# Kernel optimization log

Measured on AMD Instinct MI355X. Metric: run time of the kernel, lower is better.

## Reference

```python
import jax, jax.numpy as jnp
import numpy as np

N_ENT = 4096
N_REL = 4
F = 128
BATCH = 8192
ADJ_DENSITY = 0.01


def setup_inputs() -> dict:
    key = jax.random.key(0)
    ks = jax.random.split(key, 8)
    features = jax.random.normal(ks[0], (N_ENT, F), dtype=jnp.float32)
    # sparse binary adjacency per relation (matches count_nonzero degree normalization)
    adj = (jax.random.uniform(ks[1], (N_REL, N_ENT, N_ENT)) < ADJ_DENSITY).astype(jnp.float32)
    W1 = jax.random.normal(ks[2], (N_REL, F, F), dtype=jnp.float32)  # [R, out, in]
    W2 = jax.random.normal(ks[3], (N_REL, F, F), dtype=jnp.float32)
    # DistMult init: diagonal relation matrices (full params, as in the torch code)
    diag_vals = jax.random.normal(ks[4], (N_REL, F), dtype=jnp.float32)
    relmats = jax.vmap(jnp.diag)(diag_vals)  # [R, F, F]
    e1_idx = jax.random.randint(ks[5], (BATCH,), 0, N_ENT)
    rel_idx = jax.random.randint(ks[6], (BATCH,), 0, N_REL)
    e2_idx = jax.random.randint(ks[7], (BATCH,), 0, N_ENT)
    return {"features": features, "adj": adj, "W1": W1, "W2": W2,
            "relmats": relmats, "e1_idx": e1_idx, "rel_idx": rel_idx, "e2_idx": e2_idx}


def _conv_layer(adj, feat, W):
    # degree normalization: 1 / count_nonzero(A_r, dim=1), zeros -> 1
    deg = jnp.sum(adj != 0, axis=2).astype(feat.dtype)            # [R, N]
    inv_deg = 1.0 / jnp.where(deg == 0, 1.0, deg)                 # [R, N]
    agg = jnp.einsum('rnm,mf->rnf', adj, feat)                    # [R, N, F_in]
    y = jnp.einsum('rnf,rof->rno', agg, W)                        # [R, N, F_out] (x @ W_r.T)
    y = jnp.sum(inv_deg[:, :, None] * y, axis=0)                  # [N, F_out]
    return jax.nn.sigmoid(y)


def reference(features, adj, W1, W2, relmats, e1_idx, rel_idx, e2_idx):
    h = _conv_layer(adj, features, W1)
    h = _conv_layer(adj, h, W2)
    # DistMult scores: pred[r] = h @ M_r @ h.T  -> [R, N, N]
    pred = jnp.einsum('nf,rfg,mg->rnm', h, relmats, h)
    # per-sample scalar gather pred[rel][e1][e2]
    return pred[rel_idx, e1_idx, e2_idx]
```

## Files before the change

kernel.cpp:

```cpp
#include <hip/hip_runtime.h>
#include <hip/hip_bf16.h>

#define N_ENT 4096
#define N_REL 4
#define FDIM 128
#define KDIM 512
#define MAXNZ 128
#define BATCH 8192

__global__ __launch_bounds__(256) void k_prep(
    const float* __restrict__ W1, const float* __restrict__ W2,
    const float* __restrict__ M, const float* __restrict__ adj,
    float* __restrict__ W1T, float* __restrict__ W2T, float* __restrict__ diagM,
    unsigned short* __restrict__ cols, int* __restrict__ cnt,
    float* __restrict__ inv_deg) {
  int blk = blockIdx.x;
  if (blk < 512) {
    int id = blk * 256 + threadIdx.x;
    int which = id >> 16;
    int e = id & 65535;
    int r = e >> 14, rem = e & 16383, f = rem >> 7, o = rem & 127;
    const float* src = which ? W2 : W1;
    float* dst = which ? W2T : W1T;
    dst[e] = src[(r * FDIM + o) * FDIM + f];
    return;
  }
  if (blk < 514) {
    int idx = (blk - 512) * 256 + threadIdx.x;
    int r = idx >> 7, f = idx & 127;
    diagM[idx] = M[((size_t)(r * FDIM + f)) * FDIM + f];
    return;
  }
  int row = blk - 514;
  const float4* src = (const float4*)(adj + (size_t)row * N_ENT);
  __shared__ int lcnt;
  if (threadIdx.x == 0) lcnt = 0;
  __syncthreads();
  unsigned short* crow = cols + (size_t)row * MAXNZ;
#pragma unroll
  for (int j = 0; j < 4; ++j) {
    int vi = j * 256 + threadIdx.x;
    float4 v = src[vi];
    int base = vi * 4;
    if (v.x != 0.f) { int p = atomicAdd(&lcnt, 1); if (p < MAXNZ) crow[p] = (unsigned short)(base); }
    if (v.y != 0.f) { int p = atomicAdd(&lcnt, 1); if (p < MAXNZ) crow[p] = (unsigned short)(base + 1); }
    if (v.z != 0.f) { int p = atomicAdd(&lcnt, 1); if (p < MAXNZ) crow[p] = (unsigned short)(base + 2); }
    if (v.w != 0.f) { int p = atomicAdd(&lcnt, 1); if (p < MAXNZ) crow[p] = (unsigned short)(base + 3); }
  }
  __syncthreads();
  if (threadIdx.x == 0) {
    int c = lcnt;
    cnt[row] = c < MAXNZ ? c : MAXNZ;
    inv_deg[row] = 1.0f / (float)(c > 0 ? c : 1);
  }
}

__global__ __launch_bounds__(256) void k_gather(
    const unsigned short* __restrict__ cols, const int* __restrict__ cnt,
    const float* __restrict__ inv_deg, const float* __restrict__ feat,
    float* __restrict__ out) {
  int s = threadIdx.x >> 7;
  int node = blockIdx.x * 2 + s;
  int t = threadIdx.x & 127;
  int r = t >> 5;
  int l = t & 31;
  __shared__ unsigned short lc[2][N_REL][MAXNZ];
  int row = r * N_ENT + node;
  int c = cnt[row];
  for (int j = l; j < c; j += 32)
    lc[s][r][j] = cols[(size_t)row * MAXNZ + j];
  __syncthreads();
  float ax = 0.f, ay = 0.f, az = 0.f, aw = 0.f;
  const float* fp = feat + l * 4;
  int j = 0;
  for (; j + 4 <= c; j += 4) {
    int m0 = lc[s][r][j], m1 = lc[s][r][j + 1];
    int m2 = lc[s][r][j + 2], m3 = lc[s][r][j + 3];
    float4 v0 = *(const float4*)(fp + m0 * FDIM);
    float4 v1 = *(const float4*)(fp + m1 * FDIM);
    float4 v2 = *(const float4*)(fp + m2 * FDIM);
    float4 v3 = *(const float4*)(fp + m3 * FDIM);
    ax += v0.x + v1.x + v2.x + v3.x;
    ay += v0.y + v1.y + v2.y + v3.y;
    az += v0.z + v1.z + v2.z + v3.z;
    aw += v0.w + v1.w + v2.w + v3.w;
  }
  for (; j < c; ++j) {
    float4 v = *(const float4*)(fp + lc[s][r][j] * FDIM);
    ax += v.x; ay += v.y; az += v.z; aw += v.w;
  }
  float w = inv_deg[row];
  float4 res; res.x = ax * w; res.y = ay * w; res.z = az * w; res.w = aw * w;
  *(float4*)(out + (size_t)node * KDIM + r * FDIM + l * 4) = res;
}

__global__ __launch_bounds__(256) void k_gemm(
    const float* __restrict__ A, const float* __restrict__ B,
    float* __restrict__ C) {
  constexpr int KD = KDIM, KH = KDIM / 2, Ncol = FDIM;
  int n0 = blockIdx.x * 8;
  int o = threadIdx.x & 127;
  int half = threadIdx.x >> 7;
  const float* Ap = A + (size_t)n0 * KD + half * KH;
  const float* Bp = B + (size_t)half * KH * Ncol + o;
  float acc[8] = {0.f, 0.f, 0.f, 0.f, 0.f, 0.f, 0.f, 0.f};
#pragma unroll 2
  for (int k = 0; k < KH; k += 4) {
    float4 a0 = *(const float4*)(Ap + 0 * KD + k);
    float4 a1 = *(const float4*)(Ap + 1 * KD + k);
    float4 a2 = *(const float4*)(Ap + 2 * KD + k);
    float4 a3 = *(const float4*)(Ap + 3 * KD + k);
    float4 a4 = *(const float4*)(Ap + 4 * KD + k);
    float4 a5 = *(const float4*)(Ap + 5 * KD + k);
    float4 a6 = *(const float4*)(Ap + 6 * KD + k);
    float4 a7 = *(const float4*)(Ap + 7 * KD + k);
    float b0 = Bp[(size_t)(k + 0) * Ncol];
    float b1 = Bp[(size_t)(k + 1) * Ncol];
    float b2 = Bp[(size_t)(k + 2) * Ncol];
    float b3 = Bp[(size_t)(k + 3) * Ncol];
    acc[0] += a0.x * b0 + a0.y * b1 + a0.z * b2 + a0.w * b3;
    acc[1] += a1.x * b0 + a1.y * b1 + a1.z * b2 + a1.w * b3;
    acc[2] += a2.x * b0 + a2.y * b1 + a2.z * b2 + a2.w * b3;
    acc[3] += a3.x * b0 + a3.y * b1 + a3.z * b2 + a3.w * b3;
    acc[4] += a4.x * b0 + a4.y * b1 + a4.z * b2 + a4.w * b3;
    acc[5] += a5.x * b0 + a5.y * b1 + a5.z * b2 + a5.w * b3;
    acc[6] += a6.x * b0 + a6.y * b1 + a6.z * b2 + a6.w * b3;
    acc[7] += a7.x * b0 + a7.y * b1 + a7.z * b2 + a7.w * b3;
  }
  __shared__ float red[8][128];
  if (half) {
#pragma unroll
    for (int i = 0; i < 8; ++i) red[i][o] = acc[i];
  }
  __syncthreads();
  if (!half) {
#pragma unroll
    for (int i = 0; i < 8; ++i) {
      float v = acc[i] + red[i][o];
      v = 1.f / (1.f + __expf(-v));
      C[(size_t)(n0 + i) * Ncol + o] = v;
    }
  }
}

__global__ __launch_bounds__(256) void k_score(
    const float* __restrict__ h, const float* __restrict__ diagM,
    const int* __restrict__ e1, const int* __restrict__ rel,
    const int* __restrict__ e2, float* __restrict__ out) {
  int wave = threadIdx.x >> 6;
  int lane = threadIdx.x & 63;
  int b = blockIdx.x * 4 + wave;
  int a = e1[b], r = rel[b], c = e2[b];
  const float* hp = h + (size_t)a * FDIM;
  const float* dp = diagM + (size_t)r * FDIM;
  const float* gp = h + (size_t)c * FDIM;
  float v = hp[lane] * dp[lane] * gp[lane]
          + hp[lane + 64] * dp[lane + 64] * gp[lane + 64];
#pragma unroll
  for (int off = 32; off > 0; off >>= 1) v += __shfl_down(v, off, 64);
  if (lane == 0) out[b] = v;
}

extern "C" void kernel_launch(void* const* d_in, const int* in_sizes, int n_in,
                              void* d_out, int out_size, void* d_ws, size_t ws_size,
                              hipStream_t stream) {
  const float* feat = (const float*)d_in[0];
  const float* adj  = (const float*)d_in[1];
  const float* W1   = (const float*)d_in[2];
  const float* W2   = (const float*)d_in[3];
  const float* M    = (const float*)d_in[4];
  const int* e1     = (const int*)d_in[5];
  const int* rel    = (const int*)d_in[6];
  const int* e2     = (const int*)d_in[7];
  float* out = (float*)d_out;

  char* ws = (char*)d_ws;
  unsigned short* cols = (unsigned short*)(ws);
  int*   cnt  = (int*)  (ws + 4194304);
  float* inv  = (float*)(ws + 4259840);
  float* W1T  = (float*)(ws + 4325376);
  float* W2T  = (float*)(ws + 4587520);
  float* dM   = (float*)(ws + 4849664);
  float* agg  = (float*)(ws + 5111808);
  float* h1   = (float*)(ws + 13500416);
  float* h2   = (float*)(ws + 15597568);

  k_prep<<<514 + N_REL * N_ENT, 256, 0, stream>>>(
      W1, W2, M, adj, W1T, W2T, dM, cols, cnt, inv);

  k_gather<<<N_ENT / 2, 256, 0, stream>>>(cols, cnt, inv, feat, agg);
  k_gemm<<<N_ENT / 8, 256, 0, stream>>>(agg, W1T, h1);
  k_gather<<<N_ENT / 2, 256, 0, stream>>>(cols, cnt, inv, h1, agg);
  k_gemm<<<N_ENT / 8, 256, 0, stream>>>(agg, W2T, h2);
  k_score<<<BATCH / 4, 256, 0, stream>>>(h2, dM, e1, rel, e2, out);
}
```

Baseline: 486.5 us.

## Fuse first-layer neighbor gather into adjacency scan kernel with bitmask compaction

The adjacency-scan blocks now build a per-thread nonzero bitmask and reserve slots with one shared atomic per thread instead of one per nonzero. The compacted column indices stay in shared memory and are used immediately to aggregate the input features for that row, so the first gather kernel launch is removed. Block ordering is changed so the row blocks come first. This saves a launch and a reread of the column lists, but per-row gather now runs with only 128-dim parallelism per block, which may cut memory-level parallelism.

Measured after the change: 470.5 us. 3.3% less time.

```diff
diff --git a/kernel.cpp b/kernel.cpp
--- a/kernel.cpp
+++ b/kernel.cpp
@@ -7,52 +7,80 @@
 #define KDIM 512
 #define MAXNZ 128
 #define BATCH 8192
+#define NROWS (N_REL * N_ENT)
 
 __global__ __launch_bounds__(256) void k_prep(
     const float* __restrict__ W1, const float* __restrict__ W2,
     const float* __restrict__ M, const float* __restrict__ adj,
+    const float* __restrict__ feat,
     float* __restrict__ W1T, float* __restrict__ W2T, float* __restrict__ diagM,
     unsigned short* __restrict__ cols, int* __restrict__ cnt,
-    float* __restrict__ inv_deg) {
+    float* __restrict__ inv_deg, float* __restrict__ agg) {
   int blk = blockIdx.x;
-  if (blk < 512) {
-    int id = blk * 256 + threadIdx.x;
+  if (blk < NROWS) {
+    int row = blk;
+    int r = row >> 12;
+    int node = row & (N_ENT - 1);
+    __shared__ unsigned short sc[MAXNZ];
+    __shared__ float partial[FDIM];
+    __shared__ int lcnt;
+    if (threadIdx.x == 0) lcnt = 0;
+    __syncthreads();
+    const float4* src = (const float4*)(adj + (size_t)row * N_ENT);
+    int base = threadIdx.x * 16;
+    unsigned mask = 0;
+#pragma unroll
+    for (int q = 0; q < 4; ++q) {
+      float4 v = src[threadIdx.x * 4 + q];
+      if (v.x != 0.f) mask |= 1u << (q * 4 + 0);
+      if (v.y != 0.f) mask |= 1u << (q * 4 + 1);
+      if (v.z != 0.f) mask |= 1u << (q * 4 + 2);
+      if (v.w != 0.f) mask |= 1u << (q * 4 + 3);
+    }
+    int mycnt = __popc(mask);
+    int p = 0;
+    if (mycnt) p = atomicAdd(&lcnt, mycnt);
+    while (mask) {
+      int b = __ffs(mask) - 1;
+      mask &= mask - 1;
+      if (p < MAXNZ) sc[p] = (unsigned short)(base + b);
+      ++p;
+    }
+    __syncthreads();
+    int c = lcnt; if (c > MAXNZ) c = MAXNZ;
+    float w = 1.0f / (float)(c > 0 ? c : 1);
+    if (threadIdx.x < c) cols[(size_t)row * MAXNZ + threadIdx.x] = sc[threadIdx.x];
+    if (threadIdx.x == 0) { cnt[row] = c; inv_deg[row] = w; }
+    int f = threadIdx.x & 127;
+    int g = threadIdx.x >> 7;
+    const float* fp = feat + f;
+    float a0 = 0.f, a1 = 0.f;
+    int j = g;
+    for (; j + 2 < c; j += 4) {
+      a0 += fp[(int)sc[j] * FDIM];
+      a1 += fp[(int)sc[j + 2] * FDIM];
+    }
+    for (; j < c; j += 2) a0 += fp[(int)sc[j] * FDIM];
+    float acc = a0 + a1;
+    if (g) partial[f] = acc;
+    __syncthreads();
+    if (!g) agg[(size_t)node * KDIM + r * FDIM + f] = (acc + partial[f]) * w;
+    return;
+  }
+  int ab = blk - NROWS;
+  if (ab < 512) {
+    int id = ab * 256 + threadIdx.x;
     int which = id >> 16;
     int e = id & 65535;
-    int r = e >> 14, rem = e & 16383, f = rem >> 7, o = rem & 127;
-    const float* src = which ? W2 : W1;
+    int rr = e >> 14, rem = e & 16383, ff = rem >> 7, o = rem & 127;
+    const float* srcw = which ? W2 : W1;
     float* dst = which ? W2T : W1T;
-    dst[e] = src[(r * FDIM + o) * FDIM + f];
+    dst[e] = srcw[(rr * FDIM + o) * FDIM + ff];
     return;
   }
-  if (blk < 514) {
-    int idx = (blk - 512) * 256 + threadIdx.x;
-    int r = idx >> 7, f = idx & 127;
-    diagM[idx] = M[((size_t)(r * FDIM + f)) * FDIM + f];
-    return;
-  }
-  int row = blk - 514;
-  const float4* src = (const float4*)(adj + (size_t)row * N_ENT);
-  __shared__ int lcnt;
-  if (threadIdx.x == 0) lcnt = 0;
-  __syncthreads();
-  unsigned short* crow = cols + (size_t)row * MAXNZ;
-#pragma unroll
-  for (int j = 0; j < 4; ++j) {
-    int vi = j * 256 + threadIdx.x;
-    float4 v = src[vi];
-    int base = vi * 4;
-    if (v.x != 0.f) { int p = atomicAdd(&lcnt, 1); if (p < MAXNZ) crow[p] = (unsigned short)(base); }
-    if (v.y != 0.f) { int p = atomicAdd(&lcnt, 1); if (p < MAXNZ) crow[p] = (unsigned short)(base + 1); }
-    if (v.z != 0.f) { int p = atomicAdd(&lcnt, 1); if (p < MAXNZ) crow[p] = (unsigned short)(base + 2); }
-    if (v.w != 0.f) { int p = atomicAdd(&lcnt, 1); if (p < MAXNZ) crow[p] = (unsigned short)(base + 3); }
-  }
-  __syncthreads();
-  if (threadIdx.x == 0) {
-    int c = lcnt;
-    cnt[row] = c < MAXNZ ? c : MAXNZ;
-    inv_deg[row] = 1.0f / (float)(c > 0 ? c : 1);
-  }
+  int idx = (ab - 512) * 256 + threadIdx.x;
+  int rr = idx >> 7, ff = idx & 127;
+  diagM[idx] = M[((size_t)(rr * FDIM + ff)) * FDIM + ff];
 }
 
 __global__ __launch_bounds__(256) void k_gather(
@@ -185,10 +213,9 @@
   float* h1   = (float*)(ws + 13500416);
   float* h2   = (float*)(ws + 15597568);
 
-  k_prep<<<514 + N_REL * N_ENT, 256, 0, stream>>>(
-      W1, W2, M, adj, W1T, W2T, dM, cols, cnt, inv);
-
-  k_gather<<<N_ENT / 2, 256, 0, stream>>>(cols, cnt, inv, feat, agg);
+  k_prep<<<NROWS + 514, 256, 0, stream>>>(
+      W1, W2, M, adj, feat, W1T, W2T, dM, cols, cnt, inv, agg);
+
   k_gemm<<<N_ENT / 8, 256, 0, stream>>>(agg, W1T, h1);
   k_gather<<<N_ENT / 2, 256, 0, stream>>>(cols, cnt, inv, h1, agg);
   k_gemm<<<N_ENT / 8, 256, 0, stream>>>(agg, W2T, h2);
```
